# Optimization experiments

Hardware: AMD Instinct MI355X
Metric: run time of the kernel (lower is better)

Reference implementation:

```python
import jax, jax.numpy as jnp
import numpy as np

BITS = 4
PACK = 32 // BITS  # 8 nibbles per int32
GROUPSIZE = 128
MASK = (1 << BITS) - 1


def dequantize(qweight, qzeros, scales):
    """GPTQ dequant: W[i,o] = scales[g[i],o] * (q[i,o] - (z[g[i],o] + 1))."""
    shifts = (jnp.arange(PACK, dtype=jnp.int32) * BITS)
    # qweight: [in/8, out] packed along input dim -> [in, out]
    wq = (qweight[:, None, :] >> shifts[None, :, None]) & MASK
    wq = wq.reshape(-1, qweight.shape[1])  # [in, out] int32 in [0,15]
    # qzeros: [G, out/8] packed along output dim -> [G, out]
    zq = ((qzeros[:, :, None] >> shifts[None, None, :]) & MASK) + 1
    zq = zq.reshape(qzeros.shape[0], -1)  # [G, out]
    g_idx = jnp.arange(wq.shape[0], dtype=jnp.int32) // GROUPSIZE  # [in]
    # fp16 dequant like the CUDA/Triton GPTQ kernels
    W = (wq - zq[g_idx]).astype(jnp.float16) * scales[g_idx]
    return W  # [in, out] fp16


def setup_inputs() -> dict:
    key = jax.random.key(0)
    kx, kw, kz, ks, kb = jax.random.split(key, 5)
    in_f, out_f, groups = 4096, 4096, 4096 // GROUPSIZE
    x = jax.random.normal(kx, (8192, in_f), dtype=jnp.float16)
    qweight = jax.random.randint(kw, (in_f // PACK, out_f), 0, 2147483647, dtype=jnp.int32)
    qzeros = jax.random.randint(kz, (groups, out_f // PACK), 0, 2147483647, dtype=jnp.int32)
    scales = (jax.random.uniform(ks, (groups, out_f), dtype=jnp.float32) * 0.01 + 0.001).astype(jnp.float16)
    bias = jax.random.normal(kb, (out_f,), dtype=jnp.float16)
    return {"x": x, "qweight": qweight, "qzeros": qzeros, "scales": scales, "bias": bias}


def reference(x, qweight, qzeros, scales, bias):
    W = dequantize(qweight, qzeros, scales)  # [in, out] fp16
    # accumulate in fp32, output fp16 (matches CaiGPTQLinearOp fp16 output)
    out = jnp.matmul(x, W, preferred_element_type=jnp.float32).astype(jnp.float16)
    out = out + bias
    return out
```

## Files before the change

### kernel.cpp

```cpp
#include <hip/hip_runtime.h>

typedef _Float16 half8 __attribute__((ext_vector_type(8)));
typedef _Float16 half2v __attribute__((ext_vector_type(2)));
typedef float floatx4 __attribute__((ext_vector_type(4)));

#define K_IN 4096
#define N_OUT 4096
#define NGROUPS 32
#define BM 128
#define BN 128
#define LDA 40

__device__ __forceinline__ unsigned int pkcvt(float lo, float hi) {
    return __builtin_bit_cast(unsigned int, __builtin_amdgcn_cvt_pkrtz(lo, hi));
}

__global__ __launch_bounds__(256, 2)
void gptq_gemm_f32(const float* __restrict__ x,
                   const int*   __restrict__ qweight,
                   const int*   __restrict__ qzeros,
                   const float* __restrict__ scales,
                   const float* __restrict__ bias,
                   float*       __restrict__ out)
{
    __shared__ alignas(16) _Float16 As[2][BM * LDA];

    const int tid  = threadIdx.x;
    const int lane = tid & 63;
    const int wave = tid >> 6;
    const int l15  = lane & 15;
    const int l4   = lane >> 4;

    const int blockN = blockIdx.x * BN;
    const int blockM = blockIdx.y * BM;

    floatx4 acc[8][2] = {};

    const int srow = tid >> 2;
    const int sch  = tid & 3;
    const float* xr0 = x + (size_t)(blockM + srow) * K_IN + sch * 8;
    const float* xr1 = xr0 + (size_t)64 * K_IN;
    _Float16* lw0 = &As[0][srow * LDA + sch * 8];
    _Float16* lw1 = &As[0][(srow + 64) * LDA + sch * 8];

    int ncol[2];
#pragma unroll
    for (int j = 0; j < 2; ++j) ncol[j] = blockN + wave * 32 + j * 16 + l15;

    unsigned int zraw[2]; float sraw[2];
#pragma unroll
    for (int j = 0; j < 2; ++j) {
        zraw[j] = (unsigned int)qzeros[ncol[j] >> 3];
        sraw[j] = scales[ncol[j]];
    }
    float4 pa0 = *(const float4*)(xr0);
    float4 pa1 = *(const float4*)(xr0 + 4);
    float4 pb0 = *(const float4*)(xr1);
    float4 pb1 = *(const float4*)(xr1 + 4);
    unsigned int pq[2];
    {
        const int* qr = qweight + (size_t)l4 * N_OUT;
#pragma unroll
        for (int j = 0; j < 2; ++j) pq[j] = (unsigned int)qr[ncol[j]];
    }

    for (int g = 0; g < NGROUPS; ++g) {
        unsigned int c2u[2], s2u[2];
#pragma unroll
        for (int j = 0; j < 2; ++j) {
            const unsigned int z  = (zraw[j] >> ((ncol[j] & 7) * 4)) & 0xFu;
            const unsigned int cb = 0x6400u + z + 1u;
            c2u[j] = cb | (cb << 16);
            s2u[j] = pkcvt(sraw[j], sraw[j]);
        }
        const int gn = (g + 1 < NGROUPS) ? g + 1 : g;
#pragma unroll
        for (int j = 0; j < 2; ++j) {
            zraw[j] = (unsigned int)qzeros[gn * (N_OUT / 8) + (ncol[j] >> 3)];
            sraw[j] = scales[gn * N_OUT + ncol[j]];
        }

#pragma unroll
        for (int kk = 0; kk < 4; ++kk) {
            const int t   = g * 4 + kk;
            const int buf = t & 1;

            uint4 ra, rb;
            ra.x = pkcvt(pa0.x, pa1.x);  ra.y = pkcvt(pa0.y, pa1.y);
            ra.z = pkcvt(pa0.z, pa1.z);  ra.w = pkcvt(pa0.w, pa1.w);
            rb.x = pkcvt(pb0.x, pb1.x);  rb.y = pkcvt(pb0.y, pb1.y);
            rb.z = pkcvt(pb0.z, pb1.z);  rb.w = pkcvt(pb0.w, pb1.w);
            *(uint4*)(void*)(lw0 + buf * (BM * LDA)) = ra;
            *(uint4*)(void*)(lw1 + buf * (BM * LDA)) = rb;

            unsigned int bq[2] = {pq[0], pq[1]};

            const int t1 = (t + 1 < 4 * NGROUPS) ? t + 1 : t;
            pa0 = *(const float4*)(xr0 + t1 * 32);
            pa1 = *(const float4*)(xr0 + t1 * 32 + 4);
            pb0 = *(const float4*)(xr1 + t1 * 32);
            pb1 = *(const float4*)(xr1 + t1 * 32 + 4);
            {
                const int* qr = qweight + (size_t)(t1 * 4 + l4) * N_OUT;
#pragma unroll
                for (int j = 0; j < 2; ++j) pq[j] = (unsigned int)qr[ncol[j]];
            }

            __syncthreads();

            half8 bfrag[2];
#pragma unroll
            for (int j = 0; j < 2; ++j) {
                const unsigned int q = bq[j];
                const unsigned int r0 = (q & 0x000F000Fu)        | 0x64006400u;
                const unsigned int r1 = ((q >> 4) & 0x000F000Fu) | 0x64006400u;
                const unsigned int r2 = ((q >> 8) & 0x000F000Fu) | 0x64006400u;
                const unsigned int r3 = ((q >> 12) & 0x000F000Fu)| 0x64006400u;
                const half2v c2 = __builtin_bit_cast(half2v, c2u[j]);
                const half2v s2 = __builtin_bit_cast(half2v, s2u[j]);
                union { unsigned int u[4]; half8 h; } pk;
                pk.u[0] = __builtin_bit_cast(unsigned int,
                          (half2v)((__builtin_bit_cast(half2v, r0) - c2) * s2));
                pk.u[1] = __builtin_bit_cast(unsigned int,
                          (half2v)((__builtin_bit_cast(half2v, r1) - c2) * s2));
                pk.u[2] = __builtin_bit_cast(unsigned int,
                          (half2v)((__builtin_bit_cast(half2v, r2) - c2) * s2));
                pk.u[3] = __builtin_bit_cast(unsigned int,
                          (half2v)((__builtin_bit_cast(half2v, r3) - c2) * s2));
                bfrag[j] = pk.h;
            }

            half8 afrag[8];
#pragma unroll
            for (int i = 0; i < 8; ++i)
                afrag[i] = *(const half8*)(const void*)
                    &As[buf][(i * 16 + l15) * LDA + l4 * 8];

#pragma unroll
            for (int i = 0; i < 8; ++i)
#pragma unroll
                for (int j = 0; j < 2; ++j)
                    acc[i][j] = __builtin_amdgcn_mfma_f32_16x16x32_f16(
                        afrag[i], bfrag[j], acc[i][j], 0, 0, 0);
        }
    }

#pragma unroll
    for (int j = 0; j < 2; ++j) {
        const int n = ncol[j];
        const float bv = bias[n];
#pragma unroll
        for (int i = 0; i < 8; ++i) {
            const int m = blockM + i * 16 + l4 * 4;
#pragma unroll
            for (int r = 0; r < 4; ++r)
                out[(size_t)(m + r) * N_OUT + n] = acc[i][j][r] + bv;
        }
    }
}

extern "C" void kernel_launch(void* const* d_in, const int* in_sizes, int n_in,
                              void* d_out, int out_size, void* d_ws, size_t ws_size,
                              hipStream_t stream) {
    const float* x    = (const float*)d_in[0];
    const int*   qw   = (const int*)d_in[1];
    const int*   qz   = (const int*)d_in[2];
    const float* sc   = (const float*)d_in[3];
    const float* bias = (const float*)d_in[4];
    float*       out  = (float*)d_out;

    const int M = in_sizes[0] / K_IN;
    dim3 grid(N_OUT / BN, M / BM);
    gptq_gemm_f32<<<grid, 256, 0, stream>>>(x, qw, qz, sc, bias, out);
}
```

Baseline: 524.2 us.

## Split into fp16 pre-conversion, weight dequant pass, and plain fp16 GEMM

When the workspace is large enough, x is first converted from fp32 to fp16 and the whole weight matrix is dequantized to an fp16 K-contiguous transposed buffer, each in its own kernel. A simpler GEMM kernel then reads fp16 operands with no per-tile conversion or dequant work, and runs with a higher occupancy hint. This removes the repeated dequantization across M blocks and halves the bytes per A load. In exchange it adds two extra launches and extra global traffic: an fp16 copy of x (64MB) plus a 32MB weight buffer. The old fused kernel remains as a fallback.

```diff
diff --git a/kernel.cpp b/kernel.cpp
--- a/kernel.cpp
+++ b/kernel.cpp
@@ -15,13 +15,153 @@
     return __builtin_bit_cast(unsigned int, __builtin_amdgcn_cvt_pkrtz(lo, hi));
 }
 
+__global__ __launch_bounds__(256)
+void cvt_x_f16(const float* __restrict__ x, _Float16* __restrict__ x16) {
+    const size_t idx = ((size_t)blockIdx.x * 256 + threadIdx.x) * 8;
+    const float4 a = *(const float4*)(x + idx);
+    const float4 b = *(const float4*)(x + idx + 4);
+    uint4 u;
+    u.x = pkcvt(a.x, a.y);  u.y = pkcvt(a.z, a.w);
+    u.z = pkcvt(b.x, b.y);  u.w = pkcvt(b.z, b.w);
+    *(uint4*)(x16 + idx) = u;
+}
+
+__global__ __launch_bounds__(256)
+void dequant_wt(const int* __restrict__ qweight,
+                const int* __restrict__ qzeros,
+                const float* __restrict__ scales,
+                _Float16* __restrict__ wt)
+{
+    const int tid = threadIdx.x;
+    const int col = blockIdx.x * 64 + (tid & 63);
+    const int g   = blockIdx.y;
+    const int i   = tid >> 6;
+
+    const unsigned int zw = (unsigned int)qzeros[g * (N_OUT / 8) + (col >> 3)];
+    const unsigned int z  = (zw >> ((col & 7) * 4)) & 0xFu;
+    const unsigned int cb = 0x6400u + z + 1u;
+    const half2v c2 = __builtin_bit_cast(half2v, cb | (cb << 16));
+    const float  s  = scales[g * N_OUT + col];
+    const half2v s2 = __builtin_bit_cast(half2v, pkcvt(s, s));
+
+    const int kc0 = g * 16 + i * 4;
+#pragma unroll
+    for (int r = 0; r < 4; ++r) {
+        const unsigned int q = (unsigned int)qweight[(size_t)(kc0 + r) * N_OUT + col];
+        const unsigned int r0 = (q & 0x000F000Fu)         | 0x64006400u;
+        const unsigned int r1 = ((q >> 4) & 0x000F000Fu)  | 0x64006400u;
+        const unsigned int r2 = ((q >> 8) & 0x000F000Fu)  | 0x64006400u;
+        const unsigned int r3 = ((q >> 12) & 0x000F000Fu) | 0x64006400u;
+        unsigned int p0 = __builtin_bit_cast(unsigned int,
+                          (half2v)((__builtin_bit_cast(half2v, r0) - c2) * s2));
+        unsigned int p1 = __builtin_bit_cast(unsigned int,
+                          (half2v)((__builtin_bit_cast(half2v, r1) - c2) * s2));
+        unsigned int p2 = __builtin_bit_cast(unsigned int,
+                          (half2v)((__builtin_bit_cast(half2v, r2) - c2) * s2));
+        unsigned int p3 = __builtin_bit_cast(unsigned int,
+                          (half2v)((__builtin_bit_cast(half2v, r3) - c2) * s2));
+        uint4 nat;
+        nat.x = (p0 & 0xFFFFu) | (p1 << 16);
+        nat.y = (p2 & 0xFFFFu) | (p3 << 16);
+        nat.z = (p0 >> 16) | (p1 & 0xFFFF0000u);
+        nat.w = (p2 >> 16) | (p3 & 0xFFFF0000u);
+        *(uint4*)(wt + (size_t)col * K_IN + (kc0 + r) * 8) = nat;
+    }
+}
+
+__global__ __launch_bounds__(256, 3)
+void gemm_f16(const _Float16* __restrict__ x16,
+              const _Float16* __restrict__ wt,
+              const float* __restrict__ bias,
+              float* __restrict__ out)
+{
+    __shared__ alignas(16) _Float16 As[2][BM * LDA];
+
+    const int tid  = threadIdx.x;
+    const int lane = tid & 63;
+    const int wave = tid >> 6;
+    const int l15  = lane & 15;
+    const int l4   = lane >> 4;
+
+    const int blockN = blockIdx.x * BN;
+    const int blockM = blockIdx.y * BM;
+
+    floatx4 acc[8][2] = {};
+
+    const int srow = tid >> 2;
+    const int sch  = tid & 3;
+    const _Float16* xr0 = x16 + (size_t)(blockM + srow) * K_IN + sch * 8;
+    const _Float16* xr1 = xr0 + (size_t)64 * K_IN;
+    _Float16* lw0 = &As[0][srow * LDA + sch * 8];
+    _Float16* lw1 = &As[0][(srow + 64) * LDA + sch * 8];
+
+    int ncol[2];
+    const _Float16* wp[2];
+#pragma unroll
+    for (int j = 0; j < 2; ++j) {
+        ncol[j] = blockN + wave * 32 + j * 16 + l15;
+        wp[j]   = wt + (size_t)ncol[j] * K_IN + l4 * 8;
+    }
+
+    uint4 pa = *(const uint4*)(const void*)xr0;
+    uint4 pb = *(const uint4*)(const void*)xr1;
+    uint4 pw0 = *(const uint4*)(const void*)wp[0];
+    uint4 pw1 = *(const uint4*)(const void*)wp[1];
+
+    for (int t = 0; t < 4 * NGROUPS; ++t) {
+        const int buf = t & 1;
+
+        *(uint4*)(void*)(lw0 + buf * (BM * LDA)) = pa;
+        *(uint4*)(void*)(lw1 + buf * (BM * LDA)) = pb;
+
+        half8 bfrag[2];
+        bfrag[0] = __builtin_bit_cast(half8, pw0);
+        bfrag[1] = __builtin_bit_cast(half8, pw1);
+
+        const int t1 = (t + 1 < 4 * NGROUPS) ? t + 1 : t;
+        pa  = *(const uint4*)(const void*)(xr0 + t1 * 32);
+        pb  = *(const uint4*)(const void*)(xr1 + t1 * 32);
+        pw0 = *(const uint4*)(const void*)(wp[0] + t1 * 32);
+        pw1 = *(const uint4*)(const void*)(wp[1] + t1 * 32);
+
+        __syncthreads();
+
+        half8 afrag[8];
+#pragma unroll
+        for (int i = 0; i < 8; ++i)
+            afrag[i] = *(const half8*)(const void*)
+                &As[buf][(i * 16 + l15) * LDA + l4 * 8];
+
+#pragma unroll
+        for (int i = 0; i < 8; ++i) {
+            acc[i][0] = __builtin_amdgcn_mfma_f32_16x16x32_f16(
+                afrag[i], bfrag[0], acc[i][0], 0, 0, 0);
+            acc[i][1] = __builtin_amdgcn_mfma_f32_16x16x32_f16(
+                afrag[i], bfrag[1], acc[i][1], 0, 0, 0);
+        }
+    }
+
+#pragma unroll
+    for (int j = 0; j < 2; ++j) {
+        const int n = ncol[j];
+        const float bv = bias[n];
+#pragma unroll
+        for (int i = 0; i < 8; ++i) {
+            const int m = blockM + i * 16 + l4 * 4;
+#pragma unroll
+            for (int r = 0; r < 4; ++r)
+                out[(size_t)(m + r) * N_OUT + n] = acc[i][j][r] + bv;
+        }
+    }
+}
+
 __global__ __launch_bounds__(256, 2)
-void gptq_gemm_f32(const float* __restrict__ x,
-                   const int*   __restrict__ qweight,
-                   const int*   __restrict__ qzeros,
-                   const float* __restrict__ scales,
-                   const float* __restrict__ bias,
-                   float*       __restrict__ out)
+void gptq_gemm_fused(const float* __restrict__ x,
+                     const int*   __restrict__ qweight,
+                     const int*   __restrict__ qzeros,
+                     const float* __restrict__ scales,
+                     const float* __restrict__ bias,
+                     float*       __restrict__ out)
 {
     __shared__ alignas(16) _Float16 As[2][BM * LDA];
 
@@ -170,6 +310,19 @@
     float*       out  = (float*)d_out;
 
     const int M = in_sizes[0] / K_IN;
-    dim3 grid(N_OUT / BN, M / BM);
-    gptq_gemm_f32<<<grid, 256, 0, stream>>>(x, qw, qz, sc, bias, out);
-}
+
+    const size_t x16_bytes = (size_t)M * K_IN * sizeof(_Float16);
+    const size_t wt_bytes  = (size_t)N_OUT * K_IN * sizeof(_Float16);
+
+    if (ws_size >= x16_bytes + wt_bytes) {
+        _Float16* x16 = (_Float16*)d_ws;
+        _Float16* wtp = (_Float16*)((char*)d_ws + x16_bytes);
+
+        cvt_x_f16<<<(int)((size_t)M * K_IN / 2048), 256, 0, stream>>>(x, x16);
+        dequant_wt<<<dim3(N_OUT / 64, NGROUPS), 256, 0, stream>>>(qw, qz, sc, wtp);
+        gemm_f16<<<dim3(N_OUT / BN, M / BM), 256, 0, stream>>>(x16, wtp, bias, out);
+    } else {
+        gptq_gemm_fused<<<dim3(N_OUT / BN, M / BM), 256, 0, stream>>>(
+            x, qw, qz, sc, bias, out);
+    }
+}
```

After: 569.5 us. 1.09x slower.
